# Kernel tuning notes

Measured on AMD Instinct MI355X. Metric: run time of the kernel, lower is better.

## Reference

```python
import jax, jax.numpy as jnp
import numpy as np

EPS = 1e-12  # matches torch F.normalize default eps

def l2norm(t):
    n = jnp.linalg.norm(t, axis=-1, keepdims=True)
    return t / jnp.maximum(n, EPS)

def rotate_half(x):
    # '... (j d) -> ... j d' with j=2: split into two halves, return cat(-x2, x1)
    x1, x2 = jnp.split(x, 2, axis=-1)
    return jnp.concatenate((-x2, x1), axis=-1)

def rotary_freqs(seq_len, dim):
    inv_freq = 1.0 / (10000.0 ** (jnp.arange(0, dim, 2, dtype=jnp.float32) / dim))
    seq = jnp.arange(seq_len, dtype=jnp.float32)
    freqs = seq[:, None] * inv_freq[None, :]          # [n, d/2]
    emb = jnp.concatenate((freqs, freqs), axis=-1)    # [n, d]
    return emb[None, None]                            # [1, 1, n, d]

def apply_rotary_pos_emb(t, freqs):
    # rot_dim == dim_head here, so the pass-through slice is empty
    return t * jnp.cos(freqs) + rotate_half(t) * jnp.sin(freqs)

def setup_inputs() -> dict:
    key = jax.random.key(0)
    kq, kk, kv = jax.random.split(key, 3)
    b, h, n, d = 2, 16, 2048, 64
    q = jax.random.normal(kq, (b, h, n, d), dtype=jnp.float32)
    k = jax.random.normal(kk, (b, h, n, d), dtype=jnp.float32)
    v = jax.random.normal(kv, (b, h, n, d), dtype=jnp.float32)
    q_scale = jnp.ones((d,), dtype=jnp.float32)
    k_scale = jnp.ones((d,), dtype=jnp.float32)
    return {"q": q, "k": k, "v": v, "q_scale": q_scale, "k_scale": k_scale}

def reference(q, k, v, q_scale, k_scale):
    b, h, n, d = q.shape
    # QK RMSNorm (l2 normalize + learned per-dim scale)
    q = l2norm(q) * q_scale
    k = l2norm(k) * k_scale
    # rotary position embedding (always applied in the source module)
    freqs = rotary_freqs(n, d)
    q = apply_rotary_pos_emb(q, freqs)
    k = apply_rotary_pos_emb(k, freqs)
    # attention: explicit scores -> softmax -> values
    scale = d ** -0.5
    sim = jnp.einsum('bhid,bhjd->bhij', q, k) * scale
    attn = jax.nn.softmax(sim, axis=-1)
    out = jnp.einsum('bhij,bhjd->bhid', attn, v)
    # 'b h n d -> b n (h d)'
    return out.transpose(0, 2, 1, 3).reshape(b, n, h * d)
```

## Files before the change

### kernel.cpp

```cpp
#include <hip/hip_runtime.h>
#include <math.h>

#define BH   32
#define NSEQ 2048
#define DH   64
#define NH   16
#define LOG2E 1.44269504088896f

typedef _Float16 f16x8 __attribute__((ext_vector_type(8)));
typedef __fp16   fp16x2 __attribute__((ext_vector_type(2)));
typedef _Float16 half2v __attribute__((ext_vector_type(2)));
typedef float    f32x16v __attribute__((ext_vector_type(16)));
typedef unsigned uint2v __attribute__((ext_vector_type(2)));

#if __has_builtin(__builtin_amdgcn_exp2f)
#define EXP2F(x) __builtin_amdgcn_exp2f(x)
#else
#define EXP2F(x) exp2f(x)
#endif

static __device__ __forceinline__ unsigned pkrtz(float a, float b) {
    fp16x2 r = __builtin_amdgcn_cvt_pkrtz(a, b);
    return __builtin_bit_cast(unsigned, r);
}
static __device__ __forceinline__ unsigned packh_rne(float a, float b) {
    union { _Float16 h[2]; unsigned u; } x;
    x.h[0] = (_Float16)a; x.h[1] = (_Float16)b;
    return x.u;
}

static __device__ __forceinline__ float2 rope_cs(int pos, int p) {
    float invf_rev = EXP2F(-(float)p * (13.287712379549449f / 32.0f)) * 0.15915494309189535f;
    float rev = (float)pos * invf_rev;
    float fr = rev - floorf(rev);
    float th = fr * 6.283185307179586f;
    return make_float2(__cosf(th), __sinf(th));
}

__global__ __launch_bounds__(256) void prep_all(
    const float* __restrict__ q, const float* __restrict__ k, const float* __restrict__ v,
    const float* __restrict__ qs, const float* __restrict__ ksc,
    unsigned* __restrict__ qh, unsigned* __restrict__ kh, unsigned* __restrict__ vt2) {
    const int bid = blockIdx.x;
    const int t = threadIdx.x;
    if (bid < 16384) {
        const bool isq = bid < 8192;
        const float* in = isq ? q : k;
        const float* sc = isq ? qs : ksc;
        const float smul = isq ? 0.125f * LOG2E : 1.0f;
        const int sb = bid & 8191;
        const int w = t >> 6, lane = t & 63;
        const int c = lane & 31, hfr = lane >> 5;
        const int row = sb * 8 + w * 2 + hfr;
        float2 x2 = *(const float2*)(in + (size_t)row * DH + 2 * c);
        float ss = x2.x * x2.x + x2.y * x2.y;
        #pragma unroll
        for (int off = 16; off > 0; off >>= 1) ss += __shfl_xor(ss, off);
        float inv = 1.0f / fmaxf(sqrtf(ss), 1e-12f);
        float2 s2 = *(const float2*)(sc + 2 * c);
        float t0 = x2.x * inv * s2.x;
        float t1 = x2.y * inv * s2.y;
        float p0 = __shfl_xor(t0, 16);
        float p1 = __shfl_xor(t1, 16);
        float r0 = (c < 16) ? -p0 : p0;
        float r1 = (c < 16) ? -p1 : p1;
        int pos = row & (NSEQ - 1);
        int pp = (2 * c) & 31;
        float2 cs0 = rope_cs(pos, pp);
        float2 cs1 = rope_cs(pos, pp + 1);
        float o0 = (t0 * cs0.x + r0 * cs0.y) * smul;
        float o1 = (t1 * cs1.x + r1 * cs1.y) * smul;
        unsigned val = packh_rne(o0, o1);
        if (isq) {
            qh[row * 32 + c] = val;
        } else {
            const int rloc = row & (NSEQ - 1);
            const unsigned idx = (unsigned)((rloc >> 5) * 1024 + (c >> 3) * 256
                               + ((c >> 2) & 1) * 128 + (rloc & 31) * 4 + (c & 3));
            kh[(size_t)(row >> 11) * 65536 + idx] = val;
        }
    } else {
        const int sb = bid - 16384;
        const int kt = sb & 31, bh = sb >> 5;
        __shared__ float Lv[64 * 68];
        #pragma unroll
        for (int i = 0; i < 4; ++i) {
            int chunk = t + 256 * i;
            int r = chunk >> 4, fg = chunk & 15;
            *(float4*)&Lv[r * 68 + fg * 4] =
                *(const float4*)(v + ((size_t)bh * NSEQ + kt * 64 + r) * DH + fg * 4);
        }
        __syncthreads();
        const int d = t & 63, kg = t >> 6;
        unsigned u[8];
        #pragma unroll
        for (int j = 0; j < 8; ++j) {
            int ky = kg * 16 + 2 * j;
            u[j] = pkrtz(Lv[ky * 68 + d], Lv[(ky + 1) * 68 + d]);
        }
        const int rh = d >> 5, cc = d & 31;
        unsigned* dst = vt2 + (size_t)bh * 65536
                      + (size_t)((kt * 4 + kg) * 2 + rh) * 256 + cc * 4;
        *(uint4*)(dst)       = make_uint4(u[0], u[1], u[2], u[3]);
        *(uint4*)(dst + 128) = make_uint4(u[4], u[5], u[6], u[7]);
    }
}

static __device__ __forceinline__ f16x8 ld8(const unsigned* p) {
    return *(const f16x8*)p;
}

static __device__ __forceinline__ void load_k(f16x8 (&kd)[4], const unsigned* p) {
    #pragma unroll
    for (int ks = 0; ks < 4; ++ks) kd[ks] = ld8(p + ks * 256);
}
static __device__ __forceinline__ void load_v(f16x8 (&vd)[4], const unsigned* p) {
    #pragma unroll
    for (int kk = 0; kk < 2; ++kk)
        #pragma unroll
        for (int rh = 0; rh < 2; ++rh)
            vd[kk * 2 + rh] = ld8(p + kk * 512 + rh * 256);
}

static __device__ __forceinline__ void qk2(
    const f16x8 (&kc)[4], const f16x8 (&qf)[2][4], const f32x16v& z16,
    f32x16v& s0, f32x16v& s1)
{
    __builtin_amdgcn_s_setprio(1);
    s0 = __builtin_amdgcn_mfma_f32_32x32x16_f16(kc[0], qf[0][0], z16, 0, 0, 0);
    s1 = __builtin_amdgcn_mfma_f32_32x32x16_f16(kc[0], qf[1][0], z16, 0, 0, 0);
    #pragma unroll
    for (int ks = 1; ks < 4; ++ks) {
        s0 = __builtin_amdgcn_mfma_f32_32x32x16_f16(kc[ks], qf[0][ks], s0, 0, 0, 0);
        s1 = __builtin_amdgcn_mfma_f32_32x32x16_f16(kc[ks], qf[1][ks], s1, 0, 0, 0);
    }
    __builtin_amdgcn_s_setprio(0);
}

static __device__ __forceinline__ void pv_tile(
    f32x16v& s, const f16x8 (&vc)[4], f32x16v (&ot)[2], float& lp, int hf)
{
    #pragma unroll
    for (int r = 0; r < 16; ++r) s[r] = EXP2F(s[r]);
    #pragma unroll
    for (int kk = 0; kk < 2; ++kk) {
        unsigned P01 = pkrtz(s[kk * 8 + 0], s[kk * 8 + 1]);
        unsigned P23 = pkrtz(s[kk * 8 + 2], s[kk * 8 + 3]);
        unsigned P45 = pkrtz(s[kk * 8 + 4], s[kk * 8 + 5]);
        unsigned P67 = pkrtz(s[kk * 8 + 6], s[kk * 8 + 7]);
#if __has_builtin(__builtin_amdgcn_fdot2)
        const half2v one2 = {(_Float16)1.0f, (_Float16)1.0f};
        lp = __builtin_amdgcn_fdot2(__builtin_bit_cast(half2v, P01), one2, lp, false);
        lp = __builtin_amdgcn_fdot2(__builtin_bit_cast(half2v, P23), one2, lp, false);
        lp = __builtin_amdgcn_fdot2(__builtin_bit_cast(half2v, P45), one2, lp, false);
        lp = __builtin_amdgcn_fdot2(__builtin_bit_cast(half2v, P67), one2, lp, false);
#else
        #pragma unroll
        for (int r = 0; r < 8; ++r) lp += s[kk * 8 + r];
#endif
        union { unsigned u[4]; f16x8 v; } B;
#if __has_builtin(__builtin_amdgcn_permlane32_swap)
        uint2v r02 = __builtin_amdgcn_permlane32_swap(P01, P45, 0, 0);
        uint2v r13 = __builtin_amdgcn_permlane32_swap(P23, P67, 0, 0);
        B.u[0] = r02[0]; B.u[1] = r13[0]; B.u[2] = r02[1]; B.u[3] = r13[1];
#else
        unsigned x01 = (unsigned)__shfl_xor((int)P01, 32);
        unsigned x23 = (unsigned)__shfl_xor((int)P23, 32);
        unsigned x45 = (unsigned)__shfl_xor((int)P45, 32);
        unsigned x67 = (unsigned)__shfl_xor((int)P67, 32);
        B.u[0] = hf ? x45 : P01;
        B.u[1] = hf ? x67 : P23;
        B.u[2] = hf ? P45 : x01;
        B.u[3] = hf ? P67 : x23;
#endif
        __builtin_amdgcn_s_setprio(1);
        ot[0] = __builtin_amdgcn_mfma_f32_32x32x16_f16(vc[kk * 2 + 0], B.v, ot[0], 0, 0, 0);
        ot[1] = __builtin_amdgcn_mfma_f32_32x32x16_f16(vc[kk * 2 + 1], B.v, ot[1], 0, 0, 0);
        __builtin_amdgcn_s_setprio(0);
    }
}

static __device__ __forceinline__ void smpv2(
    f32x16v& s0, f32x16v& s1, const f16x8 (&vc)[4],
    f32x16v (&o)[2][2], float (&lp)[2], int hf)
{
    pv_tile(s0, vc, o[0], lp[0], hf);
    pv_tile(s1, vc, o[1], lp[1], hf);
}

__global__ __launch_bounds__(256, 2) void attn_kernel(
    const unsigned* __restrict__ qh, const unsigned* __restrict__ kf,
    const unsigned* __restrict__ vf, float* __restrict__ out) {

    __shared__ float Lred[128 * 33];

    const int flat = (blockIdx.x & 7) * 64 + (blockIdx.x >> 3);
    const int bh = flat >> 4, qb = flat & 15;

    const int tid = threadIdx.x;
    const int w = tid >> 6, lane = tid & 63;
    const int c = lane & 31, hf = lane >> 5;
    const int qhw = w & 1;
    const int khw = w >> 1;

    const _Float16* qbase = (const _Float16*)qh + ((size_t)bh * NSEQ + qb * 128) * DH;
    f16x8 qf[2][4];
    #pragma unroll
    for (int t = 0; t < 2; ++t)
        #pragma unroll
        for (int ks = 0; ks < 4; ++ks)
            qf[t][ks] = *(const f16x8*)(qbase + (t * 64 + qhw * 32 + c) * DH + ks * 16 + hf * 8);

    const unsigned* kfb = kf + (size_t)bh * 65536 + khw * 1024 + lane * 4;
    const unsigned* vfb = vf + (size_t)bh * 65536 + khw * 1024 + lane * 4;

    f32x16v z16;
    #pragma unroll
    for (int r = 0; r < 16; ++r) z16[r] = 0.f;

    f32x16v o[2][2];
    #pragma unroll
    for (int t = 0; t < 2; ++t)
        #pragma unroll
        for (int mt = 0; mt < 2; ++mt)
            #pragma unroll
            for (int r = 0; r < 16; ++r) o[t][mt][r] = 0.f;
    float lp[2] = {0.f, 0.f};

    f16x8 kc[4], vc[4];
    f32x16v sA0, sA1, sB0, sB1;

    load_k(kc, kfb);
    load_v(vc, vfb);
    qk2(kc, qf, z16, sA0, sA1);
    load_k(kc, kfb + 2048);

    for (int jt = 0; jt < 32; jt += 2) {
        qk2(kc, qf, z16, sB0, sB1);
        if (jt + 2 < 32) load_k(kc, kfb + (size_t)(jt + 2) * 2048);
        smpv2(sA0, sA1, vc, o, lp, hf);
        load_v(vc, vfb + (size_t)(jt + 1) * 2048);

        if (jt + 2 < 32) {
            qk2(kc, qf, z16, sA0, sA1);
            if (jt + 3 < 32) load_k(kc, kfb + (size_t)(jt + 3) * 2048);
        }
        smpv2(sB0, sB1, vc, o, lp, hf);
        if (jt + 2 < 32) load_v(vc, vfb + (size_t)(jt + 2) * 2048);
    }

    float lw[2];
    #pragma unroll
    for (int t = 0; t < 2; ++t) lw[t] = lp[t] + __shfl_xor(lp[t], 32);

    const int b = bh >> 4, h = bh & 15;
    #pragma unroll
    for (int t = 0; t < 2; ++t) {
        if (t) __syncthreads();
        if (w >= 2) {
            const int base = ((w - 2) * 64 + lane) * 33;
            f32x16v* ov = (t == 0) ? &o[0][0] : &o[1][0];
            #pragma unroll
            for (int mt = 0; mt < 2; ++mt)
                #pragma unroll
                for (int r = 0; r < 16; ++r) Lred[base + mt * 16 + r] = ov[mt][r];
            Lred[base + 32] = lw[t];
        }
        __syncthreads();
        if (w < 2) {
            const int base = (w * 64 + lane) * 33;
            f32x16v* ov = (t == 0) ? &o[0][0] : &o[1][0];
            #pragma unroll
            for (int mt = 0; mt < 2; ++mt)
                #pragma unroll
                for (int r = 0; r < 16; ++r) ov[mt][r] += Lred[base + mt * 16 + r];
            float invl = 1.0f / (lw[t] + Lred[base + 32]);
            const int pos = qb * 128 + t * 64 + w * 32 + c;
            float* obase = out + ((size_t)b * NSEQ + pos) * (NH * DH) + h * DH;
            #pragma unroll
            for (int mt = 0; mt < 2; ++mt)
                #pragma unroll
                for (int g = 0; g < 4; ++g) {
                    float4 r4 = make_float4(ov[mt][g * 4 + 0] * invl, ov[mt][g * 4 + 1] * invl,
                                            ov[mt][g * 4 + 2] * invl, ov[mt][g * 4 + 3] * invl);
                    *(float4*)(obase + mt * 32 + g * 8 + hf * 4) = r4;
                }
        }
    }
}

extern "C" void kernel_launch(void* const* d_in, const int* in_sizes, int n_in,
                              void* d_out, int out_size, void* d_ws, size_t ws_size,
                              hipStream_t stream) {
    const float* q  = (const float*)d_in[0];
    const float* k  = (const float*)d_in[1];
    const float* v  = (const float*)d_in[2];
    const float* qs = (const float*)d_in[3];
    const float* ks = (const float*)d_in[4];
    float* outp = (float*)d_out;

    unsigned* qh  = (unsigned*)d_ws;
    unsigned* kh  = qh + (size_t)BH * NSEQ * 32;
    unsigned* vt2 = kh + (size_t)BH * NSEQ * 32;

    prep_all<<<17408, 256, 0, stream>>>(q, k, v, qs, ks, qh, kh, vt2);
    attn_kernel<<<512, 256, 0, stream>>>(qh, kh, vt2, outp);
}
```

Measured before the change: 140.8 us.

## Precompute rope cos/sin table and vectorize q/k prep to 8 elements per thread

Adds a small kernel that precomputes a per-position rotary cos/sin table, so the prep kernel no longer evaluates exp2/sin/cos per element. The q/k prep now has each thread handle 8 contiguous values, using float4 loads and a uint4 store, with a 3-step shuffle reduction. This cuts the prep grid from 16384 to 4096 q/k blocks. It adds one extra kernel launch and table reads, and relies on the workspace being large enough to hold the table.

```diff
diff --git a/kernel.cpp b/kernel.cpp
--- a/kernel.cpp
+++ b/kernel.cpp
@@ -37,58 +37,82 @@
     return make_float2(__cosf(th), __sinf(th));
 }
 
+__global__ __launch_bounds__(256) void rope_tab_kernel(float4* __restrict__ tab) {
+    const int id = blockIdx.x * 256 + threadIdx.x;
+    const int pos = id >> 4, j = id & 15;
+    float2 a = rope_cs(pos, 2 * j);
+    float2 b = rope_cs(pos, 2 * j + 1);
+    tab[id] = make_float4(a.x, a.y, b.x, b.y);
+}
+
 __global__ __launch_bounds__(256) void prep_all(
     const float* __restrict__ q, const float* __restrict__ k, const float* __restrict__ v,
     const float* __restrict__ qs, const float* __restrict__ ksc,
+    const float4* __restrict__ tab,
     unsigned* __restrict__ qh, unsigned* __restrict__ kh, unsigned* __restrict__ vt2) {
     const int bid = blockIdx.x;
     const int t = threadIdx.x;
-    if (bid < 16384) {
-        const bool isq = bid < 8192;
+    if (bid < 4096) {
+        const bool isq = bid < 2048;
         const float* in = isq ? q : k;
         const float* sc = isq ? qs : ksc;
         const float smul = isq ? 0.125f * LOG2E : 1.0f;
-        const int sb = bid & 8191;
-        const int w = t >> 6, lane = t & 63;
-        const int c = lane & 31, hfr = lane >> 5;
-        const int row = sb * 8 + w * 2 + hfr;
-        float2 x2 = *(const float2*)(in + (size_t)row * DH + 2 * c);
-        float ss = x2.x * x2.x + x2.y * x2.y;
-        #pragma unroll
-        for (int off = 16; off > 0; off >>= 1) ss += __shfl_xor(ss, off);
-        float inv = 1.0f / fmaxf(sqrtf(ss), 1e-12f);
-        float2 s2 = *(const float2*)(sc + 2 * c);
-        float t0 = x2.x * inv * s2.x;
-        float t1 = x2.y * inv * s2.y;
-        float p0 = __shfl_xor(t0, 16);
-        float p1 = __shfl_xor(t1, 16);
-        float r0 = (c < 16) ? -p0 : p0;
-        float r1 = (c < 16) ? -p1 : p1;
-        int pos = row & (NSEQ - 1);
-        int pp = (2 * c) & 31;
-        float2 cs0 = rope_cs(pos, pp);
-        float2 cs1 = rope_cs(pos, pp + 1);
-        float o0 = (t0 * cs0.x + r0 * cs0.y) * smul;
-        float o1 = (t1 * cs1.x + r1 * cs1.y) * smul;
-        unsigned val = packh_rne(o0, o1);
+        const int sb = bid & 2047;
+        const int r = t >> 3, l = t & 7;
+        const int row = sb * 32 + r;
+        const int pos = row & (NSEQ - 1);
+        const float4* tb = tab + (pos << 4) + 4 * l;
+        const float4 c0 = tb[0], c1 = tb[1], c2 = tb[2], c3 = tb[3];
+        const float4 xa = *(const float4*)(in + (size_t)row * DH + 8 * l);
+        const float4 xb = *(const float4*)(in + (size_t)row * DH + 8 * l + 4);
+        float ss = xa.x * xa.x + xa.y * xa.y + xa.z * xa.z + xa.w * xa.w
+                 + xb.x * xb.x + xb.y * xb.y + xb.z * xb.z + xb.w * xb.w;
+        ss += __shfl_xor(ss, 1);
+        ss += __shfl_xor(ss, 2);
+        ss += __shfl_xor(ss, 4);
+        const float inv = 1.0f / fmaxf(sqrtf(ss), 1e-12f);
+        const float4 sa = *(const float4*)(sc + 8 * l);
+        const float4 sb4 = *(const float4*)(sc + 8 * l + 4);
+        float tv[8];
+        tv[0] = xa.x * inv * sa.x;  tv[1] = xa.y * inv * sa.y;
+        tv[2] = xa.z * inv * sa.z;  tv[3] = xa.w * inv * sa.w;
+        tv[4] = xb.x * inv * sb4.x; tv[5] = xb.y * inv * sb4.y;
+        tv[6] = xb.z * inv * sb4.z; tv[7] = xb.w * inv * sb4.w;
+        float rv[8];
+        #pragma unroll
+        for (int e = 0; e < 8; ++e) {
+            float p = __shfl_xor(tv[e], 4);
+            rv[e] = (l < 4) ? -p : p;
+        }
+        float ov[8];
+        ov[0] = (tv[0] * c0.x + rv[0] * c0.y) * smul;
+        ov[1] = (tv[1] * c0.z + rv[1] * c0.w) * smul;
+        ov[2] = (tv[2] * c1.x + rv[2] * c1.y) * smul;
+        ov[3] = (tv[3] * c1.z + rv[3] * c1.w) * smul;
+        ov[4] = (tv[4] * c2.x + rv[4] * c2.y) * smul;
+        ov[5] = (tv[5] * c2.z + rv[5] * c2.w) * smul;
+        ov[6] = (tv[6] * c3.x + rv[6] * c3.y) * smul;
+        ov[7] = (tv[7] * c3.z + rv[7] * c3.w) * smul;
+        const uint4 u4 = make_uint4(packh_rne(ov[0], ov[1]), packh_rne(ov[2], ov[3]),
+                                    packh_rne(ov[4], ov[5]), packh_rne(ov[6], ov[7]));
         if (isq) {
-            qh[row * 32 + c] = val;
+            *(uint4*)(qh + row * 32 + 4 * l) = u4;
         } else {
             const int rloc = row & (NSEQ - 1);
-            const unsigned idx = (unsigned)((rloc >> 5) * 1024 + (c >> 3) * 256
-                               + ((c >> 2) & 1) * 128 + (rloc & 31) * 4 + (c & 3));
-            kh[(size_t)(row >> 11) * 65536 + idx] = val;
+            const unsigned idx = (unsigned)((rloc >> 5) * 1024 + (l >> 1) * 256
+                               + (l & 1) * 128 + (rloc & 31) * 4);
+            *(uint4*)(kh + (size_t)(row >> 11) * 65536 + idx) = u4;
         }
     } else {
-        const int sb = bid - 16384;
+        const int sb = bid - 4096;
         const int kt = sb & 31, bh = sb >> 5;
         __shared__ float Lv[64 * 68];
         #pragma unroll
         for (int i = 0; i < 4; ++i) {
             int chunk = t + 256 * i;
-            int r = chunk >> 4, fg = chunk & 15;
-            *(float4*)&Lv[r * 68 + fg * 4] =
-                *(const float4*)(v + ((size_t)bh * NSEQ + kt * 64 + r) * DH + fg * 4);
+            int rr = chunk >> 4, fg = chunk & 15;
+            *(float4*)&Lv[rr * 68 + fg * 4] =
+                *(const float4*)(v + ((size_t)bh * NSEQ + kt * 64 + rr) * DH + fg * 4);
         }
         __syncthreads();
         const int d = t & 63, kg = t >> 6;
@@ -302,7 +326,9 @@
     unsigned* qh  = (unsigned*)d_ws;
     unsigned* kh  = qh + (size_t)BH * NSEQ * 32;
     unsigned* vt2 = kh + (size_t)BH * NSEQ * 32;
-
-    prep_all<<<17408, 256, 0, stream>>>(q, k, v, qs, ks, qh, kh, vt2);
+    float4*   tab = (float4*)(vt2 + (size_t)BH * NSEQ * 32);
+
+    rope_tab_kernel<<<128, 256, 0, stream>>>(tab);
+    prep_all<<<5120, 256, 0, stream>>>(q, k, v, qs, ks, tab, qh, kh, vt2);
     attn_kernel<<<512, 256, 0, stream>>>(qh, kh, vt2, outp);
 }
```

Measured after the change: 139.1 us, median of 3. No clear change (-1.3%).
